# Performance work log

Hardware: AMD Instinct MI355X
Metric: run time of the kernel (lower is better)

## Reference

```python
import jax, jax.numpy as jnp
import numpy as np
from functools import partial

T, B, I, H, L = 512, 256, 12, 256, 3


def setup_inputs() -> dict:
    key = jax.random.key(0)
    ks = jax.random.split(key, 1 + 4 * L + 2)
    inp = {"input": jax.random.normal(ks[0], (T, B, I), dtype=jnp.float32)}
    k = 1
    for l in range(L):
        in_dim = I if l == 0 else H
        s = 1.0 / np.sqrt(H)
        inp[f"w_ih{l}"] = jax.random.uniform(ks[k], (4 * H, in_dim), jnp.float32, -s, s); k += 1
        inp[f"w_hh{l}"] = jax.random.uniform(ks[k], (4 * H, H), jnp.float32, -s, s); k += 1
        inp[f"b_ih{l}"] = jax.random.uniform(ks[k], (4 * H,), jnp.float32, -s, s); k += 1
        inp[f"b_hh{l}"] = jax.random.uniform(ks[k], (4 * H,), jnp.float32, -s, s); k += 1
    s = 1.0 / np.sqrt(H)
    inp["w_lin"] = jax.random.uniform(ks[k], (1, H), jnp.float32, -s, s); k += 1
    inp["b_lin"] = jax.random.uniform(ks[k], (1,), jnp.float32, -s, s)
    return inp


def _lstm_layer(x, w_ih, w_hh, b_ih, b_hh):
    # x: (T, B, in_dim) -> hidden sequence (T, B, H)
    h_dim = w_hh.shape[1]
    xproj = jnp.einsum('tbi,gi->tbg', x, w_ih) + b_ih + b_hh  # (T, B, 4H)

    def step(carry, xp):
        h, c = carry
        gates = xp + h @ w_hh.T  # (B, 4H), torch gate order i,f,g,o
        i, f, g, o = jnp.split(gates, 4, axis=-1)
        i = jax.nn.sigmoid(i); f = jax.nn.sigmoid(f)
        g = jnp.tanh(g); o = jax.nn.sigmoid(o)
        c = f * c + i * g
        h = o * jnp.tanh(c)
        return (h, c), h

    bsz = x.shape[1]
    h0 = jnp.zeros((bsz, h_dim), x.dtype)
    c0 = jnp.zeros((bsz, h_dim), x.dtype)
    _, hs = jax.lax.scan(step, (h0, c0), xproj)
    return hs


def reference(input, w_ih0, w_hh0, b_ih0, b_hh0, w_ih1, w_hh1, b_ih1, b_hh1,
              w_ih2, w_hh2, b_ih2, b_hh2, w_lin, b_lin):
    params = [(w_ih0, w_hh0, b_ih0, b_hh0),
              (w_ih1, w_hh1, b_ih1, b_hh1),
              (w_ih2, w_hh2, b_ih2, b_hh2)]
    h = input
    for w_ih, w_hh, b_ih, b_hh in params:
        h = _lstm_layer(h, w_ih, w_hh, b_ih, b_hh)
    out = h @ w_lin.T + b_lin  # (T, B, 1)
    return out[..., 0]  # matches torch stack+squeeze -> (T, B)
```

## Files before the change

kernel.cpp:

```cpp
#include <hip/hip_runtime.h>

typedef _Float16 f16;
typedef _Float16 f16x4 __attribute__((ext_vector_type(4)));
typedef _Float16 f16x8 __attribute__((ext_vector_type(8)));
typedef float f32x4 __attribute__((ext_vector_type(4)));
typedef int i32x4 __attribute__((ext_vector_type(4)));

#define NSTEPS 512
#define NBATCH 256
#define HID 256
#define NL 3
#define NBG 8
#define NNW 8
#define ROWS 32
#define DRING 8
#define PITCH 260
#define THREADS 256
#define FLAGSTRIDE 16
#define NEG_INF_I (-2000000000)

#define WPACK_OFF ((size_t)65536)
#define WPACK_ELEMS ((size_t)64*16*64*8)
#define WPACK_SZB (WPACK_ELEMS*2)
#define RING_OFF (WPACK_OFF + 3*WPACK_SZB)
#define SLOT_Q 2048
#define RING_SZB ((size_t)NL*NBG*DRING*SLOT_Q*16)
#define WS_NEEDED (RING_OFF + RING_SZB)

union Gran { i32x4 v; struct { f16x4 h; int tag; int pad; } s; };

__device__ __forceinline__ float sigm(float x){ return 1.f/(1.f+__expf(-x)); }
__device__ __forceinline__ float tanh_f(float x){ return 1.f - 2.f/(1.f+__expf(2.f*x)); }

__global__ __launch_bounds__(256) void pack_weights(
    const float* __restrict__ wih0, const float* __restrict__ whh0,
    const float* __restrict__ wih1, const float* __restrict__ whh1,
    const float* __restrict__ wih2, const float* __restrict__ whh2,
    unsigned char* __restrict__ ws)
{
  int gid = blockIdx.x*256 + threadIdx.x;
  if (gid >= 3*64*16*64) return;
  int lane  = gid & 63;
  int kb    = (gid>>6) & 15;
  int nt    = (gid>>10) & 63;
  int layer = gid>>16;
  const float* whh = (layer==0)?whh0:((layer==1)?whh1:whh2);
  const float* wih = (layer==0)?wih0:((layer==1)?wih1:wih2);
  int indim = (layer==0)?12:256;
  int n  = nt*16 + (lane&15);
  int k0 = kb*32 + (lane>>4)*8;
  f16x8 v;
  #pragma unroll
  for (int e=0;e<8;++e){
    int k = k0+e;
    float x;
    if (k < HID) x = whh[n*HID + k];
    else { int ki = k-HID; x = (ki<indim)? wih[n*indim+ki] : 0.f; }
    v[e] = (f16)x;
  }
  f16* dst = (f16*)(ws + WPACK_OFF) + (size_t)layer*WPACK_ELEMS
           + ((size_t)(nt*16+kb)*64 + lane)*8;
  *(f16x8*)dst = v;
}

__global__ __launch_bounds__(THREADS, 1) void lstm_ws(
    const float* __restrict__ input,
    const float* __restrict__ bih0, const float* __restrict__ bhh0,
    const float* __restrict__ bih1, const float* __restrict__ bhh1,
    const float* __restrict__ bih2, const float* __restrict__ bhh2,
    const float* __restrict__ wlin, const float* __restrict__ blin,
    unsigned char* __restrict__ ws, float* __restrict__ out)
{
  __shared__ __attribute__((aligned(16))) f16 Hown[ROWS*PITCH];
  __shared__ __attribute__((aligned(16))) f16 Hin [ROWS*PITCH];
  __shared__ float wlinLDS[HID];

  const int tid  = threadIdx.x;
  const int w    = tid >> 6;
  const int wm   = w >> 1, wn = w & 1;
  const int lane = tid & 63;
  const int c16  = lane & 15;
  const int r0   = (lane >> 4) * 4;
  const int bid  = blockIdx.x;
  const int bg   = bid & 7;
  const int nw   = (bid >> 3) & 7;
  const int layer= bid >> 6;
  const int rowsBase = bg * ROWS;
  const int unitBase = nw * 32;
  const int arow = wm*16 + c16;

  int* flags = (int*)ws;
  int* progSelf = flags + (layer*NBG + bg)*8*FLAGSTRIDE;
  int* progUp   = (layer<2)? flags + ((layer+1)*NBG + bg)*8*FLAGSTRIDE : progSelf;

  const f16x8* wpv = (const f16x8*)((const f16*)(ws + WPACK_OFF) + (size_t)layer*WPACK_ELEMS);
  i32x4* ringSelf = (i32x4*)(ws + RING_OFF) + (size_t)((layer*NBG + bg)*DRING)*SLOT_Q;
  i32x4* ringLow  = (layer>0)? (i32x4*)(ws + RING_OFF) + (size_t)(((layer-1)*NBG + bg)*DRING)*SLOT_Q : (i32x4*)0;

  f16x8 bfr[4][16];
  #pragma unroll
  for (int G=0; G<4; ++G){
    const int nt = G*16 + nw*2 + wn;
    #pragma unroll
    for (int kb=0; kb<16; ++kb)
      bfr[G][kb] = wpv[(size_t)nt*1024 + kb*64 + lane];
  }
  if (tid < HID) wlinLDS[tid] = wlin[tid];

  const float* BIH = (layer==0)?bih0:((layer==1)?bih1:bih2);
  const float* BHH = (layer==0)?bhh0:((layer==1)?bhh1:bhh2);
  float bias[4], cst[4];
  const int unit = unitBase + wn*16 + c16;
  #pragma unroll
  for (int G=0;G<4;++G){
    int n = G*HID + unit;
    bias[G] = BIH[n] + BHH[n];
    cst[G] = 0.f;
  }
  const float bl = blin[0];
  const int rowblk = wm*4 + (lane>>4);
  const int kbv = (layer==0)? 9 : 16;

  for (int i=tid; i<ROWS*PITCH; i+=THREADS){ Hown[i]=(f16)0.f; Hin[i]=(f16)0.f; }
  __syncthreads();

  for (int t=0; t<NSTEPS; ++t){
    if (layer<2 && (t&3)==0 && t>4){
      bool act = lane < 8;
      const int* p = progUp + (lane&7)*FLAGSTRIDE;
      int need = act ? t-4 : NEG_INF_I;
      int guard = 0;
      for(;;){
        int v = act ? __hip_atomic_load(p, __ATOMIC_RELAXED, __HIP_MEMORY_SCOPE_AGENT) : 0;
        if (__all(v >= need)) break;
        if (++guard > (1<<18)) break;
        __builtin_amdgcn_s_sleep(1);
      }
    }

    if (layer == 0){
      for (int idx=tid; idx<ROWS*12; idx+=THREADS){
        int r = idx/12, i = idx - r*12;
        Hin[r*PITCH + i] = (f16)input[((size_t)t*NBATCH + rowsBase + r)*12 + i];
      }
    }

    {
      Gran go[8], gl[8];
      const i32x4* srcO = ringSelf + (size_t)((t-1)&(DRING-1))*SLOT_Q + tid;
      const i32x4* srcL = (layer>0)? ringLow + (size_t)(t&(DRING-1))*SLOT_Q + tid : (i32x4*)0;
      const bool doOwn = (t>0), doLow = (layer>0);
      int guard = 0;
      for(;;){
        if (doOwn){
          #pragma unroll
          for (int it=0; it<8; ++it)
            asm volatile("global_load_dwordx4 %0, %1, off sc0 sc1"
                         : "=v"(go[it].v) : "v"(srcO + it*THREADS) : "memory");
        }
        if (doLow){
          #pragma unroll
          for (int it=0; it<8; ++it)
            asm volatile("global_load_dwordx4 %0, %1, off sc0 sc1"
                         : "=v"(gl[it].v) : "v"(srcL + it*THREADS) : "memory");
        }
        asm volatile("s_waitcnt vmcnt(0)" ::: "memory");
        __builtin_amdgcn_sched_barrier(0);
        bool ok = true;
        if (doOwn){
          #pragma unroll
          for (int it=0; it<8; ++it) ok = ok && (go[it].s.tag >= t-1);
        }
        if (doLow){
          #pragma unroll
          for (int it=0; it<8; ++it) ok = ok && (gl[it].s.tag >= t);
        }
        if (ok || ++guard > (1<<18)) break;
      }
      if (doOwn){
        #pragma unroll
        for (int it=0; it<8; ++it){
          int i = tid + it*THREADS, rb = i>>8, un = i&255;
          f16* base = &Hown[(rb*4)*PITCH + un];
          base[0]=go[it].s.h[0]; base[PITCH]=go[it].s.h[1];
          base[2*PITCH]=go[it].s.h[2]; base[3*PITCH]=go[it].s.h[3];
        }
      }
      if (doLow){
        #pragma unroll
        for (int it=0; it<8; ++it){
          int i = tid + it*THREADS, rb = i>>8, un = i&255;
          f16* base = &Hin[(rb*4)*PITCH + un];
          base[0]=gl[it].s.h[0]; base[PITCH]=gl[it].s.h[1];
          base[2*PITCH]=gl[it].s.h[2]; base[3*PITCH]=gl[it].s.h[3];
        }
      }
    }
    __syncthreads();

    if (layer>0 && (t&3)==3 && tid==0)
      __hip_atomic_store(progSelf + nw*FLAGSTRIDE, t+1,
                         __ATOMIC_RELAXED, __HIP_MEMORY_SCOPE_AGENT);

    f32x4 acc0={bias[0],bias[0],bias[0],bias[0]};
    f32x4 acc1={bias[1],bias[1],bias[1],bias[1]};
    f32x4 acc2={bias[2],bias[2],bias[2],bias[2]};
    f32x4 acc3={bias[3],bias[3],bias[3],bias[3]};
    #pragma unroll
    for (int kb=0; kb<16; ++kb){
      if (kb < kbv){
        const f16* ap = (kb<8) ? &Hown[arow*PITCH + kb*32 + (lane>>4)*8]
                               : &Hin [arow*PITCH + (kb-8)*32 + (lane>>4)*8];
        f16x8 a = *(const f16x8*)ap;
        acc0 = __builtin_amdgcn_mfma_f32_16x16x32_f16(a, bfr[0][kb], acc0, 0,0,0);
        acc1 = __builtin_amdgcn_mfma_f32_16x16x32_f16(a, bfr[1][kb], acc1, 0,0,0);
        acc2 = __builtin_amdgcn_mfma_f32_16x16x32_f16(a, bfr[2][kb], acc2, 0,0,0);
        acc3 = __builtin_amdgcn_mfma_f32_16x16x32_f16(a, bfr[3][kb], acc3, 0,0,0);
      }
    }

    Gran gg;
    #pragma unroll
    for (int q=0;q<4;++q){
      float gi = sigm  (acc0[q]);
      float gf = sigm  (acc1[q]);
      float gg_ = tanh_f(acc2[q]);
      float go_ = sigm  (acc3[q]);
      float cv = gf*cst[q] + gi*gg_; cst[q]=cv;
      gg.s.h[q] = (f16)(go_*tanh_f(cv));
    }
    gg.s.tag = t; gg.s.pad = 0;
    {
      i32x4* dst = ringSelf + (size_t)(t&(DRING-1))*SLOT_Q + rowblk*256 + unit;
      asm volatile("global_store_dwordx4 %0, %1, off sc0 sc1"
                   :: "v"(dst), "v"(gg.v) : "memory");
    }

    if (layer==2 && t>0){
      int row = tid>>3, kc = tid&7;
      float s = 0.f;
      #pragma unroll
      for (int cc=0; cc<4; ++cc){
        f16x8 hv = *(const f16x8*)&Hown[row*PITCH + kc*32 + cc*8];
        #pragma unroll
        for (int j=0;j<8;++j) s += (float)hv[j] * wlinLDS[kc*32 + cc*8 + j];
      }
      s += __shfl_xor(s,1); s += __shfl_xor(s,2); s += __shfl_xor(s,4);
      if (kc==0) out[(size_t)(t-1)*NBATCH + rowsBase + row] = s + bl;
    }
    __syncthreads();
  }

  if (layer==2){
    Gran go[8];
    const i32x4* srcO = ringSelf + (size_t)((NSTEPS-1)&(DRING-1))*SLOT_Q + tid;
    int guard = 0;
    for(;;){
      #pragma unroll
      for (int it=0; it<8; ++it)
        asm volatile("global_load_dwordx4 %0, %1, off sc0 sc1"
                     : "=v"(go[it].v) : "v"(srcO + it*THREADS) : "memory");
      asm volatile("s_waitcnt vmcnt(0)" ::: "memory");
      __builtin_amdgcn_sched_barrier(0);
      bool ok = true;
      #pragma unroll
      for (int it=0; it<8; ++it) ok = ok && (go[it].s.tag >= NSTEPS-1);
      if (ok || ++guard > (1<<18)) break;
    }
    #pragma unroll
    for (int it=0; it<8; ++it){
      int i = tid + it*THREADS, rb = i>>8, un = i&255;
      f16* base = &Hown[(rb*4)*PITCH + un];
      base[0]=go[it].s.h[0]; base[PITCH]=go[it].s.h[1];
      base[2*PITCH]=go[it].s.h[2]; base[3*PITCH]=go[it].s.h[3];
    }
    __syncthreads();
    int row = tid>>3, kc = tid&7;
    float s = 0.f;
    #pragma unroll
    for (int cc=0; cc<4; ++cc){
      f16x8 hv = *(const f16x8*)&Hown[row*PITCH + kc*32 + cc*8];
      #pragma unroll
      for (int j=0;j<8;++j) s += (float)hv[j] * wlinLDS[kc*32 + cc*8 + j];
    }
    s += __shfl_xor(s,1); s += __shfl_xor(s,2); s += __shfl_xor(s,4);
    if (kc==0) out[(size_t)(NSTEPS-1)*NBATCH + rowsBase + row] = s + bl;
  }
}

extern "C" void kernel_launch(void* const* d_in, const int* in_sizes, int n_in,
                              void* d_out, int out_size, void* d_ws, size_t ws_size,
                              hipStream_t stream)
{
  const float* input=(const float*)d_in[0];
  const float* wih0 =(const float*)d_in[1];
  const float* whh0 =(const float*)d_in[2];
  const float* bih0 =(const float*)d_in[3];
  const float* bhh0 =(const float*)d_in[4];
  const float* wih1 =(const float*)d_in[5];
  const float* whh1 =(const float*)d_in[6];
  const float* bih1 =(const float*)d_in[7];
  const float* bhh1 =(const float*)d_in[8];
  const float* wih2 =(const float*)d_in[9];
  const float* whh2 =(const float*)d_in[10];
  const float* bih2 =(const float*)d_in[11];
  const float* bhh2 =(const float*)d_in[12];
  const float* wlin =(const float*)d_in[13];
  const float* blin =(const float*)d_in[14];
  unsigned char* ws = (unsigned char*)d_ws;
  if (ws_size < WS_NEEDED) return;

  (void)hipMemsetAsync(ws, 0, WPACK_OFF, stream);
  (void)hipMemsetAsync(ws + RING_OFF, 0xFF, RING_SZB, stream);
  hipLaunchKernelGGL(pack_weights, dim3(768), dim3(256), 0, stream,
                     wih0,whh0,wih1,whh1,wih2,whh2, ws);
  hipLaunchKernelGGL(lstm_ws, dim3(NL*NBG*NNW), dim3(THREADS), 0, stream,
                     input, bih0,bhh0,bih1,bhh1,bih2,bhh2, wlin, blin,
                     ws, (float*)d_out);
}
```

Measured before the change: 2.303 ms.

## Process two batch groups per block and halve the persistent grid

Each block now serves two batch groups (A and B) in turn within every timestep, reusing the weight fragments held in registers. The grid shrinks from 192 to 96 persistent blocks. The intent is to cut the number of blocks polling the flag and ring buffers and to reuse the loaded weights across more rows. The cost is that each block runs the sequential per-step critical path twice, which lengthens the latency-bound recurrence.

```diff
diff --git a/kernel.cpp b/kernel.cpp
--- a/kernel.cpp
+++ b/kernel.cpp
@@ -11,6 +11,7 @@
 #define HID 256
 #define NL 3
 #define NBG 8
+#define NBGP 4
 #define NNW 8
 #define ROWS 32
 #define DRING 8
@@ -80,22 +81,27 @@
   const int wm   = w >> 1, wn = w & 1;
   const int lane = tid & 63;
   const int c16  = lane & 15;
-  const int r0   = (lane >> 4) * 4;
   const int bid  = blockIdx.x;
-  const int bg   = bid & 7;
-  const int nw   = (bid >> 3) & 7;
-  const int layer= bid >> 6;
-  const int rowsBase = bg * ROWS;
+  const int bgp  = bid & 3;
+  const int nw   = (bid >> 2) & 7;
+  const int layer= bid >> 5;
+  const int bgA = bgp*2, bgB = bgp*2+1;
+  const int rowsBaseA = bgA * ROWS, rowsBaseB = bgB * ROWS;
   const int unitBase = nw * 32;
   const int arow = wm*16 + c16;
 
   int* flags = (int*)ws;
-  int* progSelf = flags + (layer*NBG + bg)*8*FLAGSTRIDE;
-  int* progUp   = (layer<2)? flags + ((layer+1)*NBG + bg)*8*FLAGSTRIDE : progSelf;
+  int* progSelfA = flags + (layer*NBG + bgA)*8*FLAGSTRIDE;
+  int* progSelfB = flags + (layer*NBG + bgB)*8*FLAGSTRIDE;
+  int* progUpA   = (layer<2)? flags + ((layer+1)*NBG + bgA)*8*FLAGSTRIDE : progSelfA;
+  int* progUpB   = (layer<2)? flags + ((layer+1)*NBG + bgB)*8*FLAGSTRIDE : progSelfB;
 
   const f16x8* wpv = (const f16x8*)((const f16*)(ws + WPACK_OFF) + (size_t)layer*WPACK_ELEMS);
-  i32x4* ringSelf = (i32x4*)(ws + RING_OFF) + (size_t)((layer*NBG + bg)*DRING)*SLOT_Q;
-  i32x4* ringLow  = (layer>0)? (i32x4*)(ws + RING_OFF) + (size_t)(((layer-1)*NBG + bg)*DRING)*SLOT_Q : (i32x4*)0;
+  i32x4* ringBase = (i32x4*)(ws + RING_OFF);
+  i32x4* ringSelfA = ringBase + (size_t)((layer*NBG + bgA)*DRING)*SLOT_Q;
+  i32x4* ringSelfB = ringBase + (size_t)((layer*NBG + bgB)*DRING)*SLOT_Q;
+  i32x4* ringLowA  = (layer>0)? ringBase + (size_t)(((layer-1)*NBG + bgA)*DRING)*SLOT_Q : (i32x4*)0;
+  i32x4* ringLowB  = (layer>0)? ringBase + (size_t)(((layer-1)*NBG + bgB)*DRING)*SLOT_Q : (i32x4*)0;
 
   f16x8 bfr[4][16];
   #pragma unroll
@@ -109,13 +115,13 @@
 
   const float* BIH = (layer==0)?bih0:((layer==1)?bih1:bih2);
   const float* BHH = (layer==0)?bhh0:((layer==1)?bhh1:bhh2);
-  float bias[4], cst[4];
+  float bias[4], cstA[4], cstB[4];
   const int unit = unitBase + wn*16 + c16;
   #pragma unroll
   for (int G=0;G<4;++G){
     int n = G*HID + unit;
     bias[G] = BIH[n] + BHH[n];
-    cst[G] = 0.f;
+    cstA[G] = 0.f; cstB[G] = 0.f;
   }
   const float bl = blin[0];
   const int rowblk = wm*4 + (lane>>4);
@@ -125,166 +131,183 @@
   __syncthreads();
 
   for (int t=0; t<NSTEPS; ++t){
-    if (layer<2 && (t&3)==0 && t>4){
-      bool act = lane < 8;
-      const int* p = progUp + (lane&7)*FLAGSTRIDE;
-      int need = act ? t-4 : NEG_INF_I;
+    #pragma unroll 1
+    for (int s=0; s<2; ++s){
+      i32x4* ringSelf = s ? ringSelfB : ringSelfA;
+      i32x4* ringLow  = s ? ringLowB  : ringLowA;
+      int* progSelf   = s ? progSelfB : progSelfA;
+      int* progUp     = s ? progUpB   : progUpA;
+      const int rowsBase = s ? rowsBaseB : rowsBaseA;
+
+      if (layer<2 && (t&3)==0 && t>4){
+        bool act = lane < 8;
+        const int* p = progUp + (lane&7)*FLAGSTRIDE;
+        int need = act ? t-4 : NEG_INF_I;
+        int guard = 0;
+        for(;;){
+          int v = act ? __hip_atomic_load(p, __ATOMIC_RELAXED, __HIP_MEMORY_SCOPE_AGENT) : 0;
+          if (__all(v >= need)) break;
+          if (++guard > (1<<18)) break;
+          __builtin_amdgcn_s_sleep(1);
+        }
+      }
+
+      if (layer == 0){
+        for (int idx=tid; idx<ROWS*12; idx+=THREADS){
+          int r = idx/12, i = idx - r*12;
+          Hin[r*PITCH + i] = (f16)input[((size_t)t*NBATCH + rowsBase + r)*12 + i];
+        }
+      }
+
+      {
+        Gran go[8], gl[8];
+        const i32x4* srcO = ringSelf + (size_t)((t-1)&(DRING-1))*SLOT_Q + tid;
+        const i32x4* srcL = (layer>0)? ringLow + (size_t)(t&(DRING-1))*SLOT_Q + tid : (i32x4*)0;
+        const bool doOwn = (t>0), doLow = (layer>0);
+        int guard = 0;
+        for(;;){
+          if (doOwn){
+            #pragma unroll
+            for (int it=0; it<8; ++it)
+              asm volatile("global_load_dwordx4 %0, %1, off sc0 sc1"
+                           : "=v"(go[it].v) : "v"(srcO + it*THREADS) : "memory");
+          }
+          if (doLow){
+            #pragma unroll
+            for (int it=0; it<8; ++it)
+              asm volatile("global_load_dwordx4 %0, %1, off sc0 sc1"
+                           : "=v"(gl[it].v) : "v"(srcL + it*THREADS) : "memory");
+          }
+          asm volatile("s_waitcnt vmcnt(0)" ::: "memory");
+          __builtin_amdgcn_sched_barrier(0);
+          bool ok = true;
+          if (doOwn){
+            #pragma unroll
+            for (int it=0; it<8; ++it) ok = ok && (go[it].s.tag >= t-1);
+          }
+          if (doLow){
+            #pragma unroll
+            for (int it=0; it<8; ++it) ok = ok && (gl[it].s.tag >= t);
+          }
+          if (ok || ++guard > (1<<18)) break;
+        }
+        if (doOwn){
+          #pragma unroll
+          for (int it=0; it<8; ++it){
+            int i = tid + it*THREADS, rb = i>>8, un = i&255;
+            f16* base = &Hown[(rb*4)*PITCH + un];
+            base[0]=go[it].s.h[0]; base[PITCH]=go[it].s.h[1];
+            base[2*PITCH]=go[it].s.h[2]; base[3*PITCH]=go[it].s.h[3];
+          }
+        }
+        if (doLow){
+          #pragma unroll
+          for (int it=0; it<8; ++it){
+            int i = tid + it*THREADS, rb = i>>8, un = i&255;
+            f16* base = &Hin[(rb*4)*PITCH + un];
+            base[0]=gl[it].s.h[0]; base[PITCH]=gl[it].s.h[1];
+            base[2*PITCH]=gl[it].s.h[2]; base[3*PITCH]=gl[it].s.h[3];
+          }
+        }
+      }
+      __syncthreads();
+
+      if (layer>0 && (t&3)==3 && tid==0)
+        __hip_atomic_store(progSelf + nw*FLAGSTRIDE, t+1,
+                           __ATOMIC_RELAXED, __HIP_MEMORY_SCOPE_AGENT);
+
+      f32x4 acc0={bias[0],bias[0],bias[0],bias[0]};
+      f32x4 acc1={bias[1],bias[1],bias[1],bias[1]};
+      f32x4 acc2={bias[2],bias[2],bias[2],bias[2]};
+      f32x4 acc3={bias[3],bias[3],bias[3],bias[3]};
+      #pragma unroll
+      for (int kb=0; kb<16; ++kb){
+        if (kb < kbv){
+          const f16* ap = (kb<8) ? &Hown[arow*PITCH + kb*32 + (lane>>4)*8]
+                                 : &Hin [arow*PITCH + (kb-8)*32 + (lane>>4)*8];
+          f16x8 a = *(const f16x8*)ap;
+          acc0 = __builtin_amdgcn_mfma_f32_16x16x32_f16(a, bfr[0][kb], acc0, 0,0,0);
+          acc1 = __builtin_amdgcn_mfma_f32_16x16x32_f16(a, bfr[1][kb], acc1, 0,0,0);
+          acc2 = __builtin_amdgcn_mfma_f32_16x16x32_f16(a, bfr[2][kb], acc2, 0,0,0);
+          acc3 = __builtin_amdgcn_mfma_f32_16x16x32_f16(a, bfr[3][kb], acc3, 0,0,0);
+        }
+      }
+
+      Gran gg;
+      #pragma unroll
+      for (int q=0;q<4;++q){
+        float gi = sigm  (acc0[q]);
+        float gf = sigm  (acc1[q]);
+        float gg_ = tanh_f(acc2[q]);
+        float go_ = sigm  (acc3[q]);
+        float cprev = s ? cstB[q] : cstA[q];
+        float cv = gf*cprev + gi*gg_;
+        if (s) cstB[q] = cv; else cstA[q] = cv;
+        gg.s.h[q] = (f16)(go_*tanh_f(cv));
+      }
+      gg.s.tag = t; gg.s.pad = 0;
+      {
+        i32x4* dst = ringSelf + (size_t)(t&(DRING-1))*SLOT_Q + rowblk*256 + unit;
+        asm volatile("global_store_dwordx4 %0, %1, off sc0 sc1"
+                     :: "v"(dst), "v"(gg.v) : "memory");
+      }
+
+      if (layer==2 && t>0){
+        int row = tid>>3, kc = tid&7;
+        float hs = 0.f;
+        #pragma unroll
+        for (int cc=0; cc<4; ++cc){
+          f16x8 hv = *(const f16x8*)&Hown[row*PITCH + kc*32 + cc*8];
+          #pragma unroll
+          for (int j=0;j<8;++j) hs += (float)hv[j] * wlinLDS[kc*32 + cc*8 + j];
+        }
+        hs += __shfl_xor(hs,1); hs += __shfl_xor(hs,2); hs += __shfl_xor(hs,4);
+        if (kc==0) out[(size_t)(t-1)*NBATCH + rowsBase + row] = hs + bl;
+      }
+      __syncthreads();
+    }
+  }
+
+  if (layer==2){
+    #pragma unroll 1
+    for (int sidx=0; sidx<2; ++sidx){
+      i32x4* ringS = sidx ? ringSelfB : ringSelfA;
+      const int rowsBaseS = sidx ? rowsBaseB : rowsBaseA;
+      Gran go[8];
+      const i32x4* srcO = ringS + (size_t)((NSTEPS-1)&(DRING-1))*SLOT_Q + tid;
       int guard = 0;
       for(;;){
-        int v = act ? __hip_atomic_load(p, __ATOMIC_RELAXED, __HIP_MEMORY_SCOPE_AGENT) : 0;
-        if (__all(v >= need)) break;
-        if (++guard > (1<<18)) break;
-        __builtin_amdgcn_s_sleep(1);
-      }
-    }
-
-    if (layer == 0){
-      for (int idx=tid; idx<ROWS*12; idx+=THREADS){
-        int r = idx/12, i = idx - r*12;
-        Hin[r*PITCH + i] = (f16)input[((size_t)t*NBATCH + rowsBase + r)*12 + i];
-      }
-    }
-
-    {
-      Gran go[8], gl[8];
-      const i32x4* srcO = ringSelf + (size_t)((t-1)&(DRING-1))*SLOT_Q + tid;
-      const i32x4* srcL = (layer>0)? ringLow + (size_t)(t&(DRING-1))*SLOT_Q + tid : (i32x4*)0;
-      const bool doOwn = (t>0), doLow = (layer>0);
-      int guard = 0;
-      for(;;){
-        if (doOwn){
-          #pragma unroll
-          for (int it=0; it<8; ++it)
-            asm volatile("global_load_dwordx4 %0, %1, off sc0 sc1"
-                         : "=v"(go[it].v) : "v"(srcO + it*THREADS) : "memory");
-        }
-        if (doLow){
-          #pragma unroll
-          for (int it=0; it<8; ++it)
-            asm volatile("global_load_dwordx4 %0, %1, off sc0 sc1"
-                         : "=v"(gl[it].v) : "v"(srcL + it*THREADS) : "memory");
-        }
+        #pragma unroll
+        for (int it=0; it<8; ++it)
+          asm volatile("global_load_dwordx4 %0, %1, off sc0 sc1"
+                       : "=v"(go[it].v) : "v"(srcO + it*THREADS) : "memory");
         asm volatile("s_waitcnt vmcnt(0)" ::: "memory");
         __builtin_amdgcn_sched_barrier(0);
         bool ok = true;
-        if (doOwn){
-          #pragma unroll
-          for (int it=0; it<8; ++it) ok = ok && (go[it].s.tag >= t-1);
-        }
-        if (doLow){
-          #pragma unroll
-          for (int it=0; it<8; ++it) ok = ok && (gl[it].s.tag >= t);
-        }
+        #pragma unroll
+        for (int it=0; it<8; ++it) ok = ok && (go[it].s.tag >= NSTEPS-1);
         if (ok || ++guard > (1<<18)) break;
       }
-      if (doOwn){
-        #pragma unroll
-        for (int it=0; it<8; ++it){
-          int i = tid + it*THREADS, rb = i>>8, un = i&255;
-          f16* base = &Hown[(rb*4)*PITCH + un];
-          base[0]=go[it].s.h[0]; base[PITCH]=go[it].s.h[1];
-          base[2*PITCH]=go[it].s.h[2]; base[3*PITCH]=go[it].s.h[3];
-        }
-      }
-      if (doLow){
-        #pragma unroll
-        for (int it=0; it<8; ++it){
-          int i = tid + it*THREADS, rb = i>>8, un = i&255;
-          f16* base = &Hin[(rb*4)*PITCH + un];
-          base[0]=gl[it].s.h[0]; base[PITCH]=gl[it].s.h[1];
-          base[2*PITCH]=gl[it].s.h[2]; base[3*PITCH]=gl[it].s.h[3];
-        }
-      }
-    }
-    __syncthreads();
-
-    if (layer>0 && (t&3)==3 && tid==0)
-      __hip_atomic_store(progSelf + nw*FLAGSTRIDE, t+1,
-                         __ATOMIC_RELAXED, __HIP_MEMORY_SCOPE_AGENT);
-
-    f32x4 acc0={bias[0],bias[0],bias[0],bias[0]};
-    f32x4 acc1={bias[1],bias[1],bias[1],bias[1]};
-    f32x4 acc2={bias[2],bias[2],bias[2],bias[2]};
-    f32x4 acc3={bias[3],bias[3],bias[3],bias[3]};
-    #pragma unroll
-    for (int kb=0; kb<16; ++kb){
-      if (kb < kbv){
-        const f16* ap = (kb<8) ? &Hown[arow*PITCH + kb*32 + (lane>>4)*8]
-                               : &Hin [arow*PITCH + (kb-8)*32 + (lane>>4)*8];
-        f16x8 a = *(const f16x8*)ap;
-        acc0 = __builtin_amdgcn_mfma_f32_16x16x32_f16(a, bfr[0][kb], acc0, 0,0,0);
-        acc1 = __builtin_amdgcn_mfma_f32_16x16x32_f16(a, bfr[1][kb], acc1, 0,0,0);
-        acc2 = __builtin_amdgcn_mfma_f32_16x16x32_f16(a, bfr[2][kb], acc2, 0,0,0);
-        acc3 = __builtin_amdgcn_mfma_f32_16x16x32_f16(a, bfr[3][kb], acc3, 0,0,0);
-      }
-    }
-
-    Gran gg;
-    #pragma unroll
-    for (int q=0;q<4;++q){
-      float gi = sigm  (acc0[q]);
-      float gf = sigm  (acc1[q]);
-      float gg_ = tanh_f(acc2[q]);
-      float go_ = sigm  (acc3[q]);
-      float cv = gf*cst[q] + gi*gg_; cst[q]=cv;
-      gg.s.h[q] = (f16)(go_*tanh_f(cv));
-    }
-    gg.s.tag = t; gg.s.pad = 0;
-    {
-      i32x4* dst = ringSelf + (size_t)(t&(DRING-1))*SLOT_Q + rowblk*256 + unit;
-      asm volatile("global_store_dwordx4 %0, %1, off sc0 sc1"
-                   :: "v"(dst), "v"(gg.v) : "memory");
-    }
-
-    if (layer==2 && t>0){
+      __syncthreads();
+      #pragma unroll
+      for (int it=0; it<8; ++it){
+        int i = tid + it*THREADS, rb = i>>8, un = i&255;
+        f16* base = &Hown[(rb*4)*PITCH + un];
+        base[0]=go[it].s.h[0]; base[PITCH]=go[it].s.h[1];
+        base[2*PITCH]=go[it].s.h[2]; base[3*PITCH]=go[it].s.h[3];
+      }
+      __syncthreads();
       int row = tid>>3, kc = tid&7;
-      float s = 0.f;
+      float hs = 0.f;
       #pragma unroll
       for (int cc=0; cc<4; ++cc){
         f16x8 hv = *(const f16x8*)&Hown[row*PITCH + kc*32 + cc*8];
         #pragma unroll
-        for (int j=0;j<8;++j) s += (float)hv[j] * wlinLDS[kc*32 + cc*8 + j];
-      }
-      s += __shfl_xor(s,1); s += __shfl_xor(s,2); s += __shfl_xor(s,4);
-      if (kc==0) out[(size_t)(t-1)*NBATCH + rowsBase + row] = s + bl;
+        for (int j=0;j<8;++j) hs += (float)hv[j] * wlinLDS[kc*32 + cc*8 + j];
+      }
+      hs += __shfl_xor(hs,1); hs += __shfl_xor(hs,2); hs += __shfl_xor(hs,4);
+      if (kc==0) out[(size_t)(NSTEPS-1)*NBATCH + rowsBaseS + row] = hs + bl;
     }
-    __syncthreads();
-  }
-
-  if (layer==2){
-    Gran go[8];
-    const i32x4* srcO = ringSelf + (size_t)((NSTEPS-1)&(DRING-1))*SLOT_Q + tid;
-    int guard = 0;
-    for(;;){
-      #pragma unroll
-      for (int it=0; it<8; ++it)
-        asm volatile("global_load_dwordx4 %0, %1, off sc0 sc1"
-                     : "=v"(go[it].v) : "v"(srcO + it*THREADS) : "memory");
-      asm volatile("s_waitcnt vmcnt(0)" ::: "memory");
-      __builtin_amdgcn_sched_barrier(0);
-      bool ok = true;
-      #pragma unroll
-      for (int it=0; it<8; ++it) ok = ok && (go[it].s.tag >= NSTEPS-1);
-      if (ok || ++guard > (1<<18)) break;
-    }
-    #pragma unroll
-    for (int it=0; it<8; ++it){
-      int i = tid + it*THREADS, rb = i>>8, un = i&255;
-      f16* base = &Hown[(rb*4)*PITCH + un];
-      base[0]=go[it].s.h[0]; base[PITCH]=go[it].s.h[1];
-      base[2*PITCH]=go[it].s.h[2]; base[3*PITCH]=go[it].s.h[3];
-    }
-    __syncthreads();
-    int row = tid>>3, kc = tid&7;
-    float s = 0.f;
-    #pragma unroll
-    for (int cc=0; cc<4; ++cc){
-      f16x8 hv = *(const f16x8*)&Hown[row*PITCH + kc*32 + cc*8];
-      #pragma unroll
-      for (int j=0;j<8;++j) s += (float)hv[j] * wlinLDS[kc*32 + cc*8 + j];
-    }
-    s += __shfl_xor(s,1); s += __shfl_xor(s,2); s += __shfl_xor(s,4);
-    if (kc==0) out[(size_t)(NSTEPS-1)*NBATCH + rowsBase + row] = s + bl;
   }
 }
 
@@ -314,7 +337,7 @@
   (void)hipMemsetAsync(ws + RING_OFF, 0xFF, RING_SZB, stream);
   hipLaunchKernelGGL(pack_weights, dim3(768), dim3(256), 0, stream,
                      wih0,whh0,wih1,whh1,wih2,whh2, ws);
-  hipLaunchKernelGGL(lstm_ws, dim3(NL*NBG*NNW), dim3(THREADS), 0, stream,
+  hipLaunchKernelGGL(lstm_ws, dim3(NL*NNW*NBGP), dim3(THREADS), 0, stream,
                      input, bih0,bhh0,bih1,bhh1,bih2,bhh2, wlin, blin,
                      ws, (float*)d_out);
 }
```

After: 4.609 ms. 100% more time.

## Halve blocks per layer: each wave computes both 16-row halves for 16 units

Applied to the files above, without the earlier changes.

Each (layer, batch group) now uses 4 blocks covering 64 hidden units instead of 8 blocks covering 32. Each wave now handles all 32 batch rows for its 16 units, issuing two MFMA chains that share the same weight fragments. The intent is to cut the number of cooperating blocks per layer, and with it the progress flags to poll and the ring traffic each block reads. The cost is twice the MFMA and activation work per wave on every step of the serial recurrence, plus higher register pressure from the extra accumulators and cell state.

```diff
diff --git a/kernel.cpp b/kernel.cpp
--- a/kernel.cpp
+++ b/kernel.cpp
@@ -11,7 +11,7 @@
 #define HID 256
 #define NL 3
 #define NBG 8
-#define NNW 8
+#define NNW 4
 #define ROWS 32
 #define DRING 8
 #define PITCH 260
@@ -77,17 +77,14 @@
 
   const int tid  = threadIdx.x;
   const int w    = tid >> 6;
-  const int wm   = w >> 1, wn = w & 1;
   const int lane = tid & 63;
   const int c16  = lane & 15;
-  const int r0   = (lane >> 4) * 4;
   const int bid  = blockIdx.x;
   const int bg   = bid & 7;
-  const int nw   = (bid >> 3) & 7;
-  const int layer= bid >> 6;
+  const int nq   = (bid >> 3) & 3;
+  const int layer= bid >> 5;
   const int rowsBase = bg * ROWS;
-  const int unitBase = nw * 32;
-  const int arow = wm*16 + c16;
+  const int unitBase = nq * 64;
 
   int* flags = (int*)ws;
   int* progSelf = flags + (layer*NBG + bg)*8*FLAGSTRIDE;
@@ -100,7 +97,7 @@
   f16x8 bfr[4][16];
   #pragma unroll
   for (int G=0; G<4; ++G){
-    const int nt = G*16 + nw*2 + wn;
+    const int nt = G*16 + nq*4 + w;
     #pragma unroll
     for (int kb=0; kb<16; ++kb)
       bfr[G][kb] = wpv[(size_t)nt*1024 + kb*64 + lane];
@@ -109,16 +106,17 @@
 
   const float* BIH = (layer==0)?bih0:((layer==1)?bih1:bih2);
   const float* BHH = (layer==0)?bhh0:((layer==1)?bhh1:bhh2);
-  float bias[4], cst[4];
-  const int unit = unitBase + wn*16 + c16;
+  float bias[4], cst0[4], cst1[4];
+  const int unit = unitBase + w*16 + c16;
   #pragma unroll
   for (int G=0;G<4;++G){
     int n = G*HID + unit;
     bias[G] = BIH[n] + BHH[n];
-    cst[G] = 0.f;
+    cst0[G] = 0.f; cst1[G] = 0.f;
   }
   const float bl = blin[0];
-  const int rowblk = wm*4 + (lane>>4);
+  const int rb0 = lane>>4;
+  const int rb1 = 4 + (lane>>4);
   const int kbv = (layer==0)? 9 : 16;
 
   for (int i=tid; i<ROWS*PITCH; i+=THREADS){ Hown[i]=(f16)0.f; Hin[i]=(f16)0.f; }
@@ -126,8 +124,8 @@
 
   for (int t=0; t<NSTEPS; ++t){
     if (layer<2 && (t&3)==0 && t>4){
-      bool act = lane < 8;
-      const int* p = progUp + (lane&7)*FLAGSTRIDE;
+      bool act = lane < 4;
+      const int* p = progUp + (lane&3)*FLAGSTRIDE;
       int need = act ? t-4 : NEG_INF_I;
       int guard = 0;
       for(;;){
@@ -199,41 +197,60 @@
     __syncthreads();
 
     if (layer>0 && (t&3)==3 && tid==0)
-      __hip_atomic_store(progSelf + nw*FLAGSTRIDE, t+1,
+      __hip_atomic_store(progSelf + nq*FLAGSTRIDE, t+1,
                          __ATOMIC_RELAXED, __HIP_MEMORY_SCOPE_AGENT);
 
-    f32x4 acc0={bias[0],bias[0],bias[0],bias[0]};
-    f32x4 acc1={bias[1],bias[1],bias[1],bias[1]};
-    f32x4 acc2={bias[2],bias[2],bias[2],bias[2]};
-    f32x4 acc3={bias[3],bias[3],bias[3],bias[3]};
+    f32x4 a00={bias[0],bias[0],bias[0],bias[0]}; f32x4 a01=a00;
+    f32x4 a10={bias[1],bias[1],bias[1],bias[1]}; f32x4 a11=a10;
+    f32x4 a20={bias[2],bias[2],bias[2],bias[2]}; f32x4 a21=a20;
+    f32x4 a30={bias[3],bias[3],bias[3],bias[3]}; f32x4 a31=a30;
     #pragma unroll
     for (int kb=0; kb<16; ++kb){
       if (kb < kbv){
-        const f16* ap = (kb<8) ? &Hown[arow*PITCH + kb*32 + (lane>>4)*8]
-                               : &Hin [arow*PITCH + (kb-8)*32 + (lane>>4)*8];
-        f16x8 a = *(const f16x8*)ap;
-        acc0 = __builtin_amdgcn_mfma_f32_16x16x32_f16(a, bfr[0][kb], acc0, 0,0,0);
-        acc1 = __builtin_amdgcn_mfma_f32_16x16x32_f16(a, bfr[1][kb], acc1, 0,0,0);
-        acc2 = __builtin_amdgcn_mfma_f32_16x16x32_f16(a, bfr[2][kb], acc2, 0,0,0);
-        acc3 = __builtin_amdgcn_mfma_f32_16x16x32_f16(a, bfr[3][kb], acc3, 0,0,0);
-      }
-    }
-
-    Gran gg;
+        const f16* base = (kb<8) ? Hown : Hin;
+        const int kk = (kb&7)*32 + (lane>>4)*8;
+        f16x8 am0 = *(const f16x8*)&base[c16*PITCH + kk];
+        f16x8 am1 = *(const f16x8*)&base[(16+c16)*PITCH + kk];
+        a00 = __builtin_amdgcn_mfma_f32_16x16x32_f16(am0, bfr[0][kb], a00, 0,0,0);
+        a01 = __builtin_amdgcn_mfma_f32_16x16x32_f16(am1, bfr[0][kb], a01, 0,0,0);
+        a10 = __builtin_amdgcn_mfma_f32_16x16x32_f16(am0, bfr[1][kb], a10, 0,0,0);
+        a11 = __builtin_amdgcn_mfma_f32_16x16x32_f16(am1, bfr[1][kb], a11, 0,0,0);
+        a20 = __builtin_amdgcn_mfma_f32_16x16x32_f16(am0, bfr[2][kb], a20, 0,0,0);
+        a21 = __builtin_amdgcn_mfma_f32_16x16x32_f16(am1, bfr[2][kb], a21, 0,0,0);
+        a30 = __builtin_amdgcn_mfma_f32_16x16x32_f16(am0, bfr[3][kb], a30, 0,0,0);
+        a31 = __builtin_amdgcn_mfma_f32_16x16x32_f16(am1, bfr[3][kb], a31, 0,0,0);
+      }
+    }
+
+    Gran gg0, gg1;
     #pragma unroll
     for (int q=0;q<4;++q){
-      float gi = sigm  (acc0[q]);
-      float gf = sigm  (acc1[q]);
-      float gg_ = tanh_f(acc2[q]);
-      float go_ = sigm  (acc3[q]);
-      float cv = gf*cst[q] + gi*gg_; cst[q]=cv;
-      gg.s.h[q] = (f16)(go_*tanh_f(cv));
-    }
-    gg.s.tag = t; gg.s.pad = 0;
+      float gi = sigm  (a00[q]);
+      float gf = sigm  (a10[q]);
+      float gG = tanh_f(a20[q]);
+      float go_ = sigm (a30[q]);
+      float cv = gf*cst0[q] + gi*gG; cst0[q]=cv;
+      gg0.s.h[q] = (f16)(go_*tanh_f(cv));
+    }
+    #pragma unroll
+    for (int q=0;q<4;++q){
+      float gi = sigm  (a01[q]);
+      float gf = sigm  (a11[q]);
+      float gG = tanh_f(a21[q]);
+      float go_ = sigm (a31[q]);
+      float cv = gf*cst1[q] + gi*gG; cst1[q]=cv;
+      gg1.s.h[q] = (f16)(go_*tanh_f(cv));
+    }
+    gg0.s.tag = t; gg0.s.pad = 0;
+    gg1.s.tag = t; gg1.s.pad = 0;
     {
-      i32x4* dst = ringSelf + (size_t)(t&(DRING-1))*SLOT_Q + rowblk*256 + unit;
+      i32x4* slot = ringSelf + (size_t)(t&(DRING-1))*SLOT_Q;
+      i32x4* dst0 = slot + rb0*256 + unit;
+      i32x4* dst1 = slot + rb1*256 + unit;
       asm volatile("global_store_dwordx4 %0, %1, off sc0 sc1"
-                   :: "v"(dst), "v"(gg.v) : "memory");
+                   :: "v"(dst0), "v"(gg0.v) : "memory");
+      asm volatile("global_store_dwordx4 %0, %1, off sc0 sc1"
+                   :: "v"(dst1), "v"(gg1.v) : "memory");
     }
 
     if (layer==2 && t>0){
```

After: 3.502 ms. 1.52x slower.
